# Kernel tuning notes

Measured on AMD Instinct MI355X. Metric: run time of the kernel, lower is better.

## Reference

```python
import jax, jax.numpy as jnp
import numpy as np

B, J, C = 8, 2048, 256
K = 32
H = 8
D = 32  # out_dim per head


def setup_inputs() -> dict:
    key = jax.random.key(0)
    k0, k1, k2, k3, k4, k5 = jax.random.split(key, 6)
    x = jax.random.normal(k0, (B, J, C), dtype=jnp.float32)
    nbr_idx = jax.random.randint(k1, (B, J, K), 0, J)
    s_in = 1.0 / np.sqrt(C)
    s_hd = 1.0 / np.sqrt(H * D)
    Wq = jax.random.uniform(k2, (C, H * D), dtype=jnp.float32, minval=-s_in, maxval=s_in)
    Wk = jax.random.uniform(k3, (C, H * D), dtype=jnp.float32, minval=-s_in, maxval=s_in)
    Wv = jax.random.uniform(k4, (C, H * D), dtype=jnp.float32, minval=-s_in, maxval=s_in)
    Wp = jax.random.uniform(k5, (H * D, D), dtype=jnp.float32, minval=-s_hd, maxval=s_hd)
    return {"x": x, "nbr_idx": nbr_idx, "Wq": Wq, "Wk": Wk, "Wv": Wv, "Wp": Wp}


def reference(x, nbr_idx, Wq, Wk, Wv, Wp):
    b, j, c = x.shape
    q = (x @ Wq).reshape(b, j, H, D)  # [B,J,H,D]
    k = (x @ Wk).reshape(b, j, H, D)
    v = (x @ Wv).reshape(b, j, H, D)
    bidx = jnp.arange(b)[:, None, None]  # [B,1,1]
    k_nbr = k[bidx, nbr_idx]  # [B,J,K,H,D]
    v_nbr = v[bidx, nbr_idx]  # [B,J,K,H,D]
    attn = jnp.einsum("bjhd,bjkhd->bjkh", q, k_nbr) / np.sqrt(D)
    attn = jax.nn.leaky_relu(attn, negative_slope=0.2)
    attn = jax.nn.softmax(attn, axis=2)  # softmax over K neighbors
    out = jnp.einsum("bjkh,bjkhd->bjhd", attn, v_nbr).reshape(b, j, H * D)
    return out @ Wp  # [B,J,D]
```

## Files before the change

### kernel.cpp

```cpp
#include <hip/hip_runtime.h>
#include <hip/hip_bf16.h>


typedef short bf16x8 __attribute__((ext_vector_type(8)));
typedef float f32x4  __attribute__((ext_vector_type(4)));
typedef float f32x2  __attribute__((ext_vector_type(2)));
typedef _Float16 h16x2 __attribute__((ext_vector_type(2)));

__device__ __forceinline__ float bf2f(unsigned short u) {
    union { unsigned int i; float f; } c; c.i = ((unsigned int)u) << 16; return c.f;
}
__device__ __forceinline__ unsigned short f2bf(float f) {
    union { float f; unsigned int i; } c; c.f = f;
    unsigned int r = c.i + 0x7FFFu + ((c.i >> 16) & 1u);
    return (unsigned short)(r >> 16);
}
__device__ __forceinline__ unsigned short f2h(float f) {
    union { _Float16 h; unsigned short u; } c; c.h = (_Float16)f;
    return c.u;
}
__device__ __forceinline__ f32x2 upk(unsigned int u) {
    union { unsigned int i; float f; } lo, hi;
    lo.i = u << 16;
    hi.i = u & 0xffff0000u;
    return (f32x2){lo.f, hi.f};
}

#if defined(__has_builtin)
#if __has_builtin(__builtin_amdgcn_fdot2)
#define HAVE_FDOT2 1
#endif
#endif
__device__ __forceinline__ float dot2acc(unsigned int a, unsigned int b, float acc) {
#ifdef HAVE_FDOT2
    union { unsigned int u; h16x2 v; } ca, cb;
    ca.u = a; cb.u = b;
    return __builtin_amdgcn_fdot2(ca.v, cb.v, acc, false);
#else
    union { unsigned int u; _Float16 h[2]; } ca, cb;
    ca.u = a; cb.u = b;
    return acc + (float)ca.h[0] * (float)cb.h[0] + (float)ca.h[1] * (float)cb.h[1];
#endif
}

__device__ __forceinline__ void gld_lds16(void* lds, const void* g) {
    __builtin_amdgcn_global_load_lds(
        (const __attribute__((address_space(1))) unsigned int*)g,
        (__attribute__((address_space(3))) unsigned int*)lds,
        16, 0, 0);
}

__global__ __launch_bounds__(256) void prep(
    const float* __restrict__ x,
    const float* __restrict__ Wq, const float* __restrict__ Wk,
    const float* __restrict__ Wv, const float* __restrict__ Wp,
    unsigned short* __restrict__ xb, unsigned short* __restrict__ Wt)
{
    const int blk = blockIdx.x, tid = threadIdx.x;
    if (blk < 4096) {
        int t = blk * 256 + tid;
        float4 f = ((const float4*)x)[t];
        ushort4 u;
        u.x = f2bf(f.x); u.y = f2bf(f.y); u.z = f2bf(f.z); u.w = f2bf(f.w);
        ((ushort4*)xb)[t] = u;
        return;
    }
    int wi = blk - 4096;
    int w = wi >> 8, n = wi & 255, t = tid;
    if (w == 0) {
        Wt[(size_t)n * 256 + t] = f2bf(Wq[(size_t)t * 256 + n]);
    } else if (w == 1) {
        Wt[(size_t)(256 + n) * 256 + t] = f2bf(Wk[(size_t)t * 256 + n]);
    } else {
        int h = n >> 5, c = n & 31;
        float acc = 0.f;
#pragma unroll
        for (int d = 0; d < 32; d++)
            acc += Wv[(size_t)t * 256 + h * 32 + d] * Wp[(size_t)(h * 32 + d) * 32 + c];
        Wt[(size_t)(512 + n) * 256 + t] = f2bf(acc);
    }
}

__global__ __launch_bounds__(256) void qkv_mfma(
    const unsigned short* __restrict__ xb,
    const unsigned short* __restrict__ Wt,
    unsigned short* __restrict__ Q, unsigned short* __restrict__ Kp,
    unsigned short* __restrict__ VP)
{
    __shared__ uint4 AlsV[1024];
    __shared__ uint4 BlsV[1024];

    const int bid = blockIdx.x;
    const int wg  = (bid & 7) * 96 + (bid >> 3);
    const int rt  = wg / 6;
    const int ct  = wg % 6;
    const int row0 = rt * 128;

    unsigned short* Y = (ct < 2) ? Q : (ct < 4) ? Kp : VP;
    const bool as_f16 = (ct < 4);
    const int  col0   = (ct & 1) * 128;

    const int tid  = threadIdx.x;
    const int w    = tid >> 6, l = tid & 63;
    const int wm   = (w >> 1) * 64, wn = (w & 1) * 64;
    const int lm   = l & 15, quad = l >> 4;
    const int swz  = (lm >> 1) & 3;

    f32x4 acc[4][4];
#pragma unroll
    for (int i = 0; i < 4; i++)
#pragma unroll
        for (int j = 0; j < 4; j++) acc[i][j] = (f32x4){0.f, 0.f, 0.f, 0.f};

    const char* Ab = (const char*)(xb + (size_t)row0 * 256);
    const char* Bb = (const char*)(Wt + (size_t)(ct * 128) * 256);

    auto stage = [&](int t, int buf) {
#pragma unroll
        for (int i = 0; i < 2; i++) {
            int cid = i * 256 + tid;
            int r   = cid >> 2;
            int cs  = cid & 3;
            int c   = cs ^ ((r >> 1) & 3);
            size_t go = (size_t)r * 512 + (size_t)t * 64 + (size_t)c * 16;
            gld_lds16((char*)AlsV + buf * 8192 + cid * 16, Ab + go);
            gld_lds16((char*)BlsV + buf * 8192 + cid * 16, Bb + go);
        }
    };

    stage(0, 0);
    __syncthreads();

    int cur = 0;
    for (int t = 0; t < 8; ++t) {
        if (t < 7) stage(t + 1, cur ^ 1);

        const char* Abase = (const char*)AlsV + cur * 8192;
        const char* Bbase = (const char*)BlsV + cur * 8192;
        bf16x8 a[4], b[4];
#pragma unroll
        for (int tm = 0; tm < 4; tm++) {
            int R = wm + tm * 16 + lm;
            a[tm] = *(const bf16x8*)(Abase + R * 64 + ((quad ^ swz) << 4));
        }
#pragma unroll
        for (int tn = 0; tn < 4; tn++) {
            int R = wn + tn * 16 + lm;
            b[tn] = *(const bf16x8*)(Bbase + R * 64 + ((quad ^ swz) << 4));
        }
#pragma unroll
        for (int tm = 0; tm < 4; tm++)
#pragma unroll
            for (int tn = 0; tn < 4; tn++)
                acc[tm][tn] = __builtin_amdgcn_mfma_f32_16x16x32_bf16(
                    a[tm], b[tn], acc[tm][tn], 0, 0, 0);

        __syncthreads();
        cur ^= 1;
    }

#pragma unroll
    for (int tm = 0; tm < 4; tm++) {
        int rbase = row0 + wm + tm * 16 + quad * 4;
#pragma unroll
        for (int tn = 0; tn < 4; tn++) {
            int col = col0 + wn + tn * 16 + lm;
            if (as_f16) {
#pragma unroll
                for (int r = 0; r < 4; r++)
                    Y[(size_t)(rbase + r) * 256 + col] = f2h(acc[tm][tn][r]);
            } else {
#pragma unroll
                for (int r = 0; r < 4; r++)
                    Y[(size_t)(rbase + r) * 256 + col] = f2bf(acc[tm][tn][r]);
            }
        }
    }
}

__global__ __launch_bounds__(256) void attn_wave(
    const unsigned short* __restrict__ qb,
    const unsigned short* __restrict__ kb,
    const unsigned short* __restrict__ vp,
    const int*            __restrict__ nbr,
    float*                __restrict__ out)
{
    const int beta = blockIdx.x;
    const int b    = beta & 7;
    const int jt   = beta >> 3;
    const int tid  = threadIdx.x;
    const int w    = tid >> 6;
    const int l    = tid & 63;
    const int lh   = l & 31;
    const int h5   = l >> 5;
    const int bj   = (b << 11) + jt * 4 + w;
    const size_t bbase = (size_t)b << 19;
    const int* nrow = nbr + (size_t)bj * 32;

    int ko = nrow[lh] << 8;
    int koff[16];
#pragma unroll
    for (int r = 0; r < 16; r++) koff[r] = __shfl(ko, 2 * r + h5);

    uint4 qu = *(const uint4*)(qb + (size_t)bj * 256 + lh * 8);

    uint4 kr[16];
#pragma unroll
    for (int r = 0; r < 16; r++)
        kr[r] = *(const uint4*)(kb + bbase + koff[r] + lh * 8);

    float s[16];
#pragma unroll
    for (int r = 0; r < 16; r++) {
        float a = 0.f;
        a = dot2acc(kr[r].x, qu.x, a);
        a = dot2acc(kr[r].y, qu.y, a);
        a = dot2acc(kr[r].z, qu.z, a);
        a = dot2acc(kr[r].w, qu.w, a);
        a += __shfl_xor(a, 1);
        a += __shfl_xor(a, 2);
        a *= 0.17677669529663687f;
        s[r] = (a > 0.f) ? a : 0.2f * a;
    }

    uint4 vr[16];
#pragma unroll
    for (int r = 0; r < 16; r++)
        vr[r] = *(const uint4*)(vp + bbase + koff[r] + lh * 8);

    float m = s[0];
#pragma unroll
    for (int r = 1; r < 16; r++) m = fmaxf(m, s[r]);
    m = fmaxf(m, __shfl_xor(m, 32));
    float sum = 0.f;
#pragma unroll
    for (int r = 0; r < 16; r++) { s[r] = __expf(s[r] - m); sum += s[r]; }
    sum += __shfl_xor(sum, 32);
    const float inv = 1.0f / sum;
#pragma unroll
    for (int r = 0; r < 16; r++) s[r] *= inv;

    f32x2 a0 = (f32x2){0.f, 0.f}, a1 = a0, a2 = a0, a3 = a0;
#pragma unroll
    for (int r = 0; r < 16; r++) {
        const f32x2 w2 = (f32x2){s[r], s[r]};
        a0 += upk(vr[r].x) * w2;
        a1 += upk(vr[r].y) * w2;
        a2 += upk(vr[r].z) * w2;
        a3 += upk(vr[r].w) * w2;
    }

    float o[8] = {a0.x, a0.y, a1.x, a1.y, a2.x, a2.y, a3.x, a3.y};
#pragma unroll
    for (int i = 0; i < 8; i++) o[i] += __shfl_xor(o[i], 32);
#pragma unroll
    for (int i = 0; i < 8; i++) o[i] += __shfl_xor(o[i], 4);
#pragma unroll
    for (int i = 0; i < 8; i++) o[i] += __shfl_xor(o[i], 8);
#pragma unroll
    for (int i = 0; i < 8; i++) o[i] += __shfl_xor(o[i], 16);

    if (l < 4) {
        float* op = out + (size_t)bj * 32 + l * 8;
        *(float4*)(op)     = make_float4(o[0], o[1], o[2], o[3]);
        *(float4*)(op + 4) = make_float4(o[4], o[5], o[6], o[7]);
    }
}

__global__ __launch_bounds__(256) void fused_all(
    const float* __restrict__ X, const int* __restrict__ nbr,
    const float* __restrict__ Wq, const float* __restrict__ Wk,
    const float* __restrict__ Wv, const float* __restrict__ Wp,
    float* __restrict__ out)
{
    __shared__ float xr[256], qrow[256], xn[256];
    __shared__ float vn[32][256];
    __shared__ int   nb[32];
    __shared__ float sc[32][8], pwv[32][8];
    __shared__ float sp[256], hd[256];
    __shared__ float red[8][32];

    const int bj = blockIdx.x, b = bj >> 11, tid = threadIdx.x;

    xr[tid] = X[(size_t)bj * 256 + tid];
    if (tid < 32) nb[tid] = nbr[(size_t)bj * 32 + tid];
    __syncthreads();

    {
        float acc = 0.f;
#pragma unroll 8
        for (int c = 0; c < 256; c++) acc += xr[c] * Wq[(size_t)c * 256 + tid];
        qrow[tid] = acc;
    }
    __syncthreads();

    for (int i = 0; i < 32; i++) {
        size_t r = (size_t)(b * 2048 + nb[i]);
        xn[tid] = X[r * 256 + tid];
        __syncthreads();
        float ka = 0.f, va = 0.f;
#pragma unroll 8
        for (int c = 0; c < 256; c++) {
            float xc = xn[c];
            ka += xc * Wk[(size_t)c * 256 + tid];
            va += xc * Wv[(size_t)c * 256 + tid];
        }
        vn[i][tid] = va;
        sp[tid] = qrow[tid] * ka;
        __syncthreads();
        if (tid < 8) {
            float s = 0.f;
#pragma unroll
            for (int d = 0; d < 32; d++) s += sp[tid * 32 + d];
            s *= 0.17677669529663687f;
            s = (s > 0.f) ? s : 0.2f * s;
            sc[i][tid] = s;
        }
        __syncthreads();
    }

    {
        const int h = tid & 7, kk = tid >> 3;
        float mx = -1e30f;
#pragma unroll
        for (int i = 0; i < 32; i++) mx = fmaxf(mx, sc[i][h]);
        float ssum = 0.f;
#pragma unroll
        for (int i = 0; i < 32; i++) ssum += __expf(sc[i][h] - mx);
        pwv[kk][h] = __expf(sc[kk][h] - mx) / ssum;
    }
    __syncthreads();

    {
        const int h2 = tid >> 5;
        float acc = 0.f;
#pragma unroll 8
        for (int i = 0; i < 32; i++) acc += pwv[i][h2] * vn[i][tid];
        hd[tid] = acc;
    }
    __syncthreads();

    {
        const int c = tid & 31, ch = tid >> 5;
        float p = 0.f;
#pragma unroll
        for (int i = 0; i < 32; i++) { int r = ch * 32 + i; p += hd[r] * Wp[r * 32 + c]; }
        red[ch][c] = p;
    }
    __syncthreads();

    if (tid < 32) {
        float o = 0.f;
#pragma unroll
        for (int i = 0; i < 8; i++) o += red[i][tid];
        out[(size_t)bj * 32 + tid] = o;
    }
}

extern "C" void kernel_launch(void* const* d_in, const int* in_sizes, int n_in,
                              void* d_out, int out_size, void* d_ws, size_t ws_size,
                              hipStream_t stream) {
    const float* x   = (const float*)d_in[0];
    const int*   nbr = (const int*)d_in[1];
    const float* Wq  = (const float*)d_in[2];
    const float* Wk  = (const float*)d_in[3];
    const float* Wv  = (const float*)d_in[4];
    const float* Wp  = (const float*)d_in[5];
    float*       out = (float*)d_out;

    const size_t ME   = (size_t)16384 * 256;
    const size_t need = (4 * ME + 3 * 65536) * sizeof(unsigned short);

    if (ws_size >= need) {
        unsigned short* q  = (unsigned short*)d_ws;
        unsigned short* k  = q + ME;
        unsigned short* vp = k + ME;
        unsigned short* xb = vp + ME;
        unsigned short* Wt = xb + ME;

        prep<<<4096 + 768, 256, 0, stream>>>(x, Wq, Wk, Wv, Wp, xb, Wt);
        qkv_mfma<<<768, 256, 0, stream>>>(xb, Wt, q, k, vp);
        attn_wave<<<4096, 256, 0, stream>>>(q, k, vp, nbr, out);
    } else {
        fused_all<<<16384, 256, 0, stream>>>(x, nbr, Wq, Wk, Wv, Wp, out);
    }
}
```

Before: 118.1 us.

## Fuse x bf16 conversion into QKV GEMM and stage epilogue through LDS

Drops the separate pass that converted x to bf16 in the prep kernel. The QKV GEMM now loads fp32 x into registers, converts it, and writes bf16 tiles to LDS while the MFMAs for the current tile run. This removes a full write and read of the bf16 copy of x. The output epilogue now goes through a swizzled LDS buffer so the results are written with coalesced 16-byte stores instead of scattered 2-byte stores. In exchange, the A-side global loads are twice as large because x stays fp32, each of the 6 column tiles converts the same x rows again, and register pressure rises.

```diff
diff --git a/kernel.cpp b/kernel.cpp
--- a/kernel.cpp
+++ b/kernel.cpp
@@ -7,9 +7,6 @@
 typedef float f32x2  __attribute__((ext_vector_type(2)));
 typedef _Float16 h16x2 __attribute__((ext_vector_type(2)));
 
-__device__ __forceinline__ float bf2f(unsigned short u) {
-    union { unsigned int i; float f; } c; c.i = ((unsigned int)u) << 16; return c.f;
-}
 __device__ __forceinline__ unsigned short f2bf(float f) {
     union { float f; unsigned int i; } c; c.f = f;
     unsigned int r = c.i + 0x7FFFu + ((c.i >> 16) & 1u);
@@ -51,22 +48,12 @@
 }
 
 __global__ __launch_bounds__(256) void prep(
-    const float* __restrict__ x,
     const float* __restrict__ Wq, const float* __restrict__ Wk,
     const float* __restrict__ Wv, const float* __restrict__ Wp,
-    unsigned short* __restrict__ xb, unsigned short* __restrict__ Wt)
+    unsigned short* __restrict__ Wt)
 {
-    const int blk = blockIdx.x, tid = threadIdx.x;
-    if (blk < 4096) {
-        int t = blk * 256 + tid;
-        float4 f = ((const float4*)x)[t];
-        ushort4 u;
-        u.x = f2bf(f.x); u.y = f2bf(f.y); u.z = f2bf(f.z); u.w = f2bf(f.w);
-        ((ushort4*)xb)[t] = u;
-        return;
-    }
-    int wi = blk - 4096;
-    int w = wi >> 8, n = wi & 255, t = tid;
+    const int wi = blockIdx.x, tid = threadIdx.x;
+    const int w = wi >> 8, n = wi & 255, t = tid;
     if (w == 0) {
         Wt[(size_t)n * 256 + t] = f2bf(Wq[(size_t)t * 256 + n]);
     } else if (w == 1) {
@@ -82,13 +69,12 @@
 }
 
 __global__ __launch_bounds__(256) void qkv_mfma(
-    const unsigned short* __restrict__ xb,
+    const float* __restrict__ x,
     const unsigned short* __restrict__ Wt,
     unsigned short* __restrict__ Q, unsigned short* __restrict__ Kp,
     unsigned short* __restrict__ VP)
 {
-    __shared__ uint4 AlsV[1024];
-    __shared__ uint4 BlsV[1024];
+    __shared__ uint4 LDSbuf[2048];
 
     const int bid = blockIdx.x;
     const int wg  = (bid & 7) * 96 + (bid >> 3);
@@ -112,31 +98,60 @@
 #pragma unroll
         for (int j = 0; j < 4; j++) acc[i][j] = (f32x4){0.f, 0.f, 0.f, 0.f};
 
-    const char* Ab = (const char*)(xb + (size_t)row0 * 256);
-    const char* Bb = (const char*)(Wt + (size_t)(ct * 128) * 256);
-
-    auto stage = [&](int t, int buf) {
+    const float* xA = x + (size_t)row0 * 256;
+    const char*  Bb = (const char*)(Wt + (size_t)(ct * 128) * 256);
+
+    int ar[2], ac[2];
+#pragma unroll
+    for (int i = 0; i < 2; i++) {
+        int cid = i * 256 + tid;
+        ar[i] = cid >> 2;
+        ac[i] = (cid & 3) ^ ((ar[i] >> 1) & 3);
+    }
+
+    float4 areg[2][2];
+    auto a_issue = [&](int t) {
+#pragma unroll
+        for (int i = 0; i < 2; i++) {
+            const float* s = xA + (size_t)ar[i] * 256 + t * 32 + ac[i] * 8;
+            areg[i][0] = *(const float4*)(s);
+            areg[i][1] = *(const float4*)(s + 4);
+        }
+    };
+    auto a_write = [&](int buf) {
 #pragma unroll
         for (int i = 0; i < 2; i++) {
             int cid = i * 256 + tid;
-            int r   = cid >> 2;
-            int cs  = cid & 3;
-            int c   = cs ^ ((r >> 1) & 3);
-            size_t go = (size_t)r * 512 + (size_t)t * 64 + (size_t)c * 16;
-            gld_lds16((char*)AlsV + buf * 8192 + cid * 16, Ab + go);
-            gld_lds16((char*)BlsV + buf * 8192 + cid * 16, Bb + go);
+            uint4 v;
+            v.x = (unsigned int)f2bf(areg[i][0].x) | ((unsigned int)f2bf(areg[i][0].y) << 16);
+            v.y = (unsigned int)f2bf(areg[i][0].z) | ((unsigned int)f2bf(areg[i][0].w) << 16);
+            v.z = (unsigned int)f2bf(areg[i][1].x) | ((unsigned int)f2bf(areg[i][1].y) << 16);
+            v.w = (unsigned int)f2bf(areg[i][1].z) | ((unsigned int)f2bf(areg[i][1].w) << 16);
+            *(uint4*)((char*)LDSbuf + buf * 8192 + cid * 16) = v;
         }
     };
-
-    stage(0, 0);
+    auto b_stage = [&](int t, int buf) {
+#pragma unroll
+        for (int i = 0; i < 2; i++) {
+            int cid = i * 256 + tid;
+            int r = cid >> 2, cs = cid & 3;
+            int c = cs ^ ((r >> 1) & 3);
+            gld_lds16((char*)LDSbuf + 16384 + buf * 8192 + cid * 16,
+                      Bb + (size_t)r * 512 + (size_t)t * 64 + (size_t)c * 16);
+        }
+    };
+
+    a_issue(0);
+    b_stage(0, 0);
+    a_write(0);
     __syncthreads();
 
     int cur = 0;
     for (int t = 0; t < 8; ++t) {
-        if (t < 7) stage(t + 1, cur ^ 1);
-
-        const char* Abase = (const char*)AlsV + cur * 8192;
-        const char* Bbase = (const char*)BlsV + cur * 8192;
+        if (t < 7) { a_issue(t + 1); b_stage(t + 1, cur ^ 1); }
+
+        const char* Abase = (const char*)LDSbuf + cur * 8192;
+        const char* Bbase = (const char*)LDSbuf + 16384 + cur * 8192;
         bf16x8 a[4], b[4];
 #pragma unroll
         for (int tm = 0; tm < 4; tm++) {
@@ -155,26 +170,32 @@
                 acc[tm][tn] = __builtin_amdgcn_mfma_f32_16x16x32_bf16(
                     a[tm], b[tn], acc[tm][tn], 0, 0, 0);
 
+        if (t < 7) a_write(cur ^ 1);
+
         __syncthreads();
         cur ^= 1;
     }
 
-#pragma unroll
-    for (int tm = 0; tm < 4; tm++) {
-        int rbase = row0 + wm + tm * 16 + quad * 4;
-#pragma unroll
-        for (int tn = 0; tn < 4; tn++) {
-            int col = col0 + wn + tn * 16 + lm;
-            if (as_f16) {
-#pragma unroll
-                for (int r = 0; r < 4; r++)
-                    Y[(size_t)(rbase + r) * 256 + col] = f2h(acc[tm][tn][r]);
-            } else {
-#pragma unroll
-                for (int r = 0; r < 4; r++)
-                    Y[(size_t)(rbase + r) * 256 + col] = f2bf(acc[tm][tn][r]);
+    unsigned short* ep = (unsigned short*)LDSbuf;
+#pragma unroll
+    for (int tm = 0; tm < 4; tm++)
+#pragma unroll
+        for (int tn = 0; tn < 4; tn++)
+#pragma unroll
+            for (int r = 0; r < 4; r++) {
+                int rr  = wm + tm * 16 + quad * 4 + r;
+                int col = wn + tn * 16 + lm;
+                unsigned short u = as_f16 ? f2h(acc[tm][tn][r]) : f2bf(acc[tm][tn][r]);
+                int byte = rr * 256 + ((((col >> 3) ^ (rr & 15))) << 4) + (col & 7) * 2;
+                *(unsigned short*)((char*)ep + byte) = u;
             }
-        }
+    __syncthreads();
+#pragma unroll
+    for (int it = 0; it < 8; it++) {
+        int id = it * 256 + tid;
+        int r2 = id >> 4, cc = id & 15;
+        uint4 v = *(const uint4*)((char*)ep + r2 * 256 + ((cc ^ (r2 & 15)) << 4));
+        *(uint4*)(Y + (size_t)(row0 + r2) * 256 + col0 + cc * 8) = v;
     }
 }
 
@@ -369,17 +390,17 @@
     float*       out = (float*)d_out;
 
     const size_t ME   = (size_t)16384 * 256;
-    const size_t need = (4 * ME + 3 * 65536) * sizeof(unsigned short);
+    const size_t WTE  = (size_t)768 * 256;
+    const size_t need = (3 * ME + WTE) * sizeof(unsigned short);
 
     if (ws_size >= need) {
         unsigned short* q  = (unsigned short*)d_ws;
         unsigned short* k  = q + ME;
         unsigned short* vp = k + ME;
-        unsigned short* xb = vp + ME;
-        unsigned short* Wt = xb + ME;
-
-        prep<<<4096 + 768, 256, 0, stream>>>(x, Wq, Wk, Wv, Wp, xb, Wt);
-        qkv_mfma<<<768, 256, 0, stream>>>(xb, Wt, q, k, vp);
+        unsigned short* Wt = vp + ME;
+
+        prep<<<768, 256, 0, stream>>>(Wq, Wk, Wv, Wp, Wt);
+        qkv_mfma<<<768, 256, 0, stream>>>(x, Wt, q, k, vp);
         attn_wave<<<4096, 256, 0, stream>>>(q, k, vp, nbr, out);
     } else {
         fused_all<<<16384, 256, 0, stream>>>(x, nbr, Wq, Wk, Wv, Wp, out);
```

New measurement: 114.6 us. 1.03x faster.
